# Performance work log

Hardware: AMD Instinct MI355X
Metric: run time of the kernel (lower is better)

The kernel has to match this reference:

```python
import jax, jax.numpy as jnp
import numpy as np

C_M, C_Z, H, C = 256, 128, 8, 32  # msa emb, pair emb, heads, head channels
S, R = 128, 256                   # MSA rows, residues


def layer_norm(x, gamma, beta, eps=1e-5):
    mu = jnp.mean(x, axis=-1, keepdims=True)
    var = jnp.var(x, axis=-1, keepdims=True)
    return (x - mu) * jax.lax.rsqrt(var + eps) * gamma + beta


def setup_inputs() -> dict:
    key = jax.random.key(0)
    ks = jax.random.split(key, 12)
    sc_m = 1.0 / np.sqrt(C_M)
    sc_z = 1.0 / np.sqrt(C_Z)
    sc_hc = 1.0 / np.sqrt(H * C)
    return {
        "msa_rep": jax.random.normal(ks[0], (S, R, C_M), dtype=jnp.float32),
        "pair_rep": jax.random.normal(ks[1], (R, R, C_Z), dtype=jnp.float32),
        "ln_msa_g": jnp.ones((C_M,), jnp.float32),
        "ln_msa_b": jnp.zeros((C_M,), jnp.float32),
        "ln_pair_g": jnp.ones((C_Z,), jnp.float32),
        "ln_pair_b": jnp.zeros((C_Z,), jnp.float32),
        "w_q": jax.random.normal(ks[2], (C_M, H, C), jnp.float32) * sc_m,
        "w_k": jax.random.normal(ks[3], (C_M, H, C), jnp.float32) * sc_m,
        "w_v": jax.random.normal(ks[4], (C_M, H, C), jnp.float32) * sc_m,
        "w_g": jax.random.normal(ks[5], (C_M, H, C), jnp.float32) * sc_m,
        "b_g": jnp.zeros((H, C), jnp.float32),
        "w_b": jax.random.normal(ks[6], (C_Z, H), jnp.float32) * sc_z,
        "b_b": jnp.zeros((H,), jnp.float32),
        "w_o": jax.random.normal(ks[7], (H, C, C_M), jnp.float32) * sc_hc,
        "b_o": jnp.zeros((C_M,), jnp.float32),
    }


def reference(msa_rep, pair_rep, ln_msa_g, ln_msa_b, ln_pair_g, ln_pair_b,
              w_q, w_k, w_v, w_g, b_g, w_b, b_b, w_o, b_o):
    m = layer_norm(msa_rep, ln_msa_g, ln_msa_b)                 # [S,R,C_M]
    q = jnp.einsum('src,chd->srhd', m, w_q)                     # [S,R,H,C]
    k = jnp.einsum('src,chd->srhd', m, w_k)
    v = jnp.einsum('src,chd->srhd', m, w_v)
    gates = jax.nn.sigmoid(jnp.einsum('src,chd->srhd', m, w_g) + b_g)
    # pair bias: [R,R,H] -> [H,R,R]
    z = layer_norm(pair_rep, ln_pair_g, ln_pair_b)
    b = jnp.einsum('ijc,ch->hij', z, w_b) + b_b[:, None, None]  # [H,R,R]
    logits = jnp.einsum('sqhd,skhd->shqk', q, k) / np.sqrt(C)   # [S,H,R,R]
    logits = logits + b[None]
    w = jax.nn.softmax(logits, axis=-1)
    o = jnp.einsum('shqk,skhd->sqhd', w, v)                     # [S,R,H,C]
    o = gates * o
    out = jnp.einsum('srhd,hdc->src', o, w_o) + b_o             # [S,R,C_M]
    return out
```

## Files before the change

kernel.cpp:

```cpp
#include <hip/hip_runtime.h>
#include <hip/hip_bf16.h>

#define S_DIM 128
#define R_DIM 256
#define CM 256
#define CZ 128
#define H_DIM 8
#define C_DIM 32

typedef short bf16x8 __attribute__((ext_vector_type(8)));
typedef float f32x4 __attribute__((ext_vector_type(4)));

__device__ inline ushort f2b(float f) {
  __hip_bfloat16 b = __float2bfloat16(f);
  return *(ushort*)&b;
}
__device__ inline float b2f(ushort u) {
  __hip_bfloat16 b = *(__hip_bfloat16*)&u;
  return __bfloat162float(b);
}

__device__ __forceinline__ void gld_lds16(const ushort* g, ushort* l) {
  __builtin_amdgcn_global_load_lds(
      (const __attribute__((address_space(1))) unsigned int*)g,
      (__attribute__((address_space(3))) unsigned int*)l, 16, 0, 0);
}

__global__ __launch_bounds__(256) void wt_kernel(
    const float* __restrict__ wq, const float* __restrict__ wk,
    const float* __restrict__ wv, const float* __restrict__ wg,
    const float* __restrict__ wo, ushort* __restrict__ Wt5) {
  __shared__ float t[64][65];
  int z = blockIdx.z;
  const float* W = (z == 0) ? wq : (z == 1) ? wk : (z == 2) ? wv
                   : (z == 3) ? wg : wo;
  ushort* Wt = Wt5 + (size_t)z * 65536;
  int tid = threadIdx.x;
  int r = tid >> 2, c4 = (tid & 3) * 16;
  int rowBase = blockIdx.y * 64, colBase = blockIdx.x * 64;
#pragma unroll
  for (int j = 0; j < 16; ++j)
    t[r][c4 + j] = W[(size_t)(rowBase + r) * 256 + colBase + c4 + j];
  __syncthreads();
#pragma unroll
  for (int j = 0; j < 16; ++j)
    Wt[(size_t)(colBase + r) * 256 + rowBase + c4 + j] = f2b(t[c4 + j][r]);
}

__global__ __launch_bounds__(256) void ln_msa_kernel(
    const float* __restrict__ x, const float* __restrict__ g,
    const float* __restrict__ b, ushort* __restrict__ m) {
  int lane = threadIdx.x & 63, w = threadIdx.x >> 6;
  int row = blockIdx.x * 4 + w;
  const float* xp = x + (size_t)row * CM + lane * 4;
  float4 v = *(const float4*)xp;
  float s1 = v.x + v.y + v.z + v.w;
  float s2 = v.x * v.x + v.y * v.y + v.z * v.z + v.w * v.w;
#pragma unroll
  for (int off = 32; off; off >>= 1) {
    s1 += __shfl_xor(s1, off, 64);
    s2 += __shfl_xor(s2, off, 64);
  }
  float mean = s1 * (1.0f / CM);
  float rstd = rsqrtf(s2 * (1.0f / CM) - mean * mean + 1e-5f);
  float4 gv = *(const float4*)(g + lane * 4);
  float4 bv = *(const float4*)(b + lane * 4);
  ushort4 o;
  o.x = f2b((v.x - mean) * rstd * gv.x + bv.x);
  o.y = f2b((v.y - mean) * rstd * gv.y + bv.y);
  o.z = f2b((v.z - mean) * rstd * gv.z + bv.z);
  o.w = f2b((v.w - mean) * rstd * gv.w + bv.w);
  *(ushort4*)(m + (size_t)row * CM + lane * 4) = o;
}

__global__ __launch_bounds__(256) void pair_bias_kernel(
    const float* __restrict__ z, const float* __restrict__ g,
    const float* __restrict__ b, const float* __restrict__ w_b,
    const float* __restrict__ b_b, float* __restrict__ bias) {
  __shared__ float wbs[CZ][8];
  __shared__ float gs[CZ], bs[CZ];
  int tid = threadIdx.x;
  if (tid < CZ) { gs[tid] = g[tid]; bs[tid] = b[tid]; }
  for (int i = tid; i < CZ * 8; i += 256) wbs[i >> 3][i & 7] = w_b[i];
  __syncthreads();
  int q = tid & 3;
  int row = blockIdx.x * 64 + (tid >> 2);
  const float* zp = z + (size_t)row * CZ + q * 32;
  float4 v[8];
#pragma unroll
  for (int j = 0; j < 8; ++j) v[j] = *(const float4*)(zp + j * 4);
  float s1 = 0.f, s2 = 0.f;
#pragma unroll
  for (int j = 0; j < 8; ++j) {
    s1 += v[j].x + v[j].y + v[j].z + v[j].w;
    s2 += v[j].x * v[j].x + v[j].y * v[j].y + v[j].z * v[j].z +
          v[j].w * v[j].w;
  }
  s1 += __shfl_xor(s1, 1, 64);
  s2 += __shfl_xor(s2, 1, 64);
  s1 += __shfl_xor(s1, 2, 64);
  s2 += __shfl_xor(s2, 2, 64);
  float mean = s1 * (1.0f / CZ);
  float var = s2 * (1.0f / CZ) - mean * mean;
  float rstd = rsqrtf(var + 1e-5f);
  float acc[8] = {};
#pragma unroll
  for (int j = 0; j < 8; ++j) {
    float e[4] = {v[j].x, v[j].y, v[j].z, v[j].w};
#pragma unroll
    for (int u = 0; u < 4; ++u) {
      int c = q * 32 + j * 4 + u;
      float zn = (e[u] - mean) * rstd * gs[c] + bs[c];
#pragma unroll
      for (int h = 0; h < 8; ++h) acc[h] += zn * wbs[c][h];
    }
  }
#pragma unroll
  for (int h = 0; h < 8; ++h) {
    acc[h] += __shfl_xor(acc[h], 1, 64);
    acc[h] += __shfl_xor(acc[h], 2, 64);
  }
  int h0 = q * 2;
  bias[(size_t)h0 * (R_DIM * R_DIM) + row] = acc[h0] + b_b[h0];
  bias[(size_t)(h0 + 1) * (R_DIM * R_DIM) + row] = acc[h0 + 1] + b_b[h0 + 1];
}

__global__ __launch_bounds__(256) void proj_mfma(
    const ushort* __restrict__ M, const ushort* __restrict__ Wt5,
    const float* __restrict__ b_g, ushort* __restrict__ qb,
    ushort* __restrict__ kb2, ushort* __restrict__ vb,
    ushort* __restrict__ gb) {
  __shared__ ushort As[128 * 64];
  __shared__ ushort Bs[128 * 64];
  int tid = threadIdx.x, lane = tid & 63, wid = tid >> 6;
  int lr = lane & 15, lg = lane >> 4;
  int rowBase = blockIdx.x * 128;
  int colBase = blockIdx.y * 128;
  int proj = colBase >> 8;
  int sc = (lane & 7) ^ ((lane >> 3) & 7);
  const ushort* Ag =
      M + (size_t)(rowBase + wid * 32 + (lane >> 3)) * 256 + sc * 8;
  const ushort* Bg =
      Wt5 + (size_t)(colBase + wid * 32 + (lane >> 3)) * 256 + sc * 8;
  ushort* Asl = As + wid * (32 * 64);
  ushort* Bsl = Bs + wid * (32 * 64);
  int wr = wid >> 1, wc = wid & 1;
  int sx = (lr & 7) * 8;
  f32x4 zf = {0.f, 0.f, 0.f, 0.f};
  f32x4 acc[4][4];
#pragma unroll
  for (int i = 0; i < 4; ++i)
#pragma unroll
    for (int j = 0; j < 4; ++j) acc[i][j] = zf;

  for (int kb = 0; kb < 4; ++kb) {
    if (kb) __syncthreads();
#pragma unroll
    for (int c = 0; c < 4; ++c) {
      gld_lds16(Ag + kb * 64 + c * (8 * 256), Asl + c * (8 * 64));
      gld_lds16(Bg + kb * 64 + c * (8 * 256), Bsl + c * (8 * 64));
    }
    __syncthreads();
#pragma unroll
    for (int kk = 0; kk < 2; ++kk) {
      bf16x8 a[4], b[4];
#pragma unroll
      for (int mf = 0; mf < 4; ++mf)
        a[mf] = *(const bf16x8*)&As[(wr * 64 + mf * 16 + lr) * 64 +
                                    ((kk * 32 + lg * 8) ^ sx)];
#pragma unroll
      for (int nf = 0; nf < 4; ++nf)
        b[nf] = *(const bf16x8*)&Bs[(wc * 64 + nf * 16 + lr) * 64 +
                                    ((kk * 32 + lg * 8) ^ sx)];
#pragma unroll
      for (int mf = 0; mf < 4; ++mf)
#pragma unroll
        for (int nf = 0; nf < 4; ++nf)
          acc[mf][nf] = __builtin_amdgcn_mfma_f32_16x16x32_bf16(
              a[mf], b[nf], acc[mf][nf], 0, 0, 0);
    }
  }
#pragma unroll
  for (int mf = 0; mf < 4; ++mf)
#pragma unroll
    for (int nf = 0; nf < 4; ++nf)
#pragma unroll
      for (int r = 0; r < 4; ++r) {
        int row = rowBase + wr * 64 + mf * 16 + lg * 4 + r;
        int col = (colBase & 255) + wc * 64 + nf * 16 + lr;
        int s = row >> 8, rr = row & 255, h = col >> 5, d = col & 31;
        size_t oidx = ((size_t)((s * H_DIM + h) * R_DIM + rr)) * C_DIM + d;
        float val = acc[mf][nf][r];
        if (proj == 0)
          qb[oidx] = f2b(val * 0.17677669529663687f);
        else if (proj == 1)
          kb2[oidx] = f2b(val);
        else if (proj == 2)
          vb[oidx] = f2b(val);
        else {
          val = 1.f / (1.f + __expf(-(val + b_g[col])));
          gb[oidx] = f2b(val);
        }
      }
}

__global__ __launch_bounds__(512, 4) void attn_mfma(
    const ushort* __restrict__ q, const ushort* __restrict__ k,
    const ushort* __restrict__ v, const ushort* __restrict__ g,
    const float* __restrict__ bias, ushort* __restrict__ ob) {
  __shared__ ushort Vt[32][264];
  __shared__ ushort Pl[8][32][72];
  int blk = blockIdx.x;
  int s = blk >> 3, h = blk & 7;
  int tid = threadIdx.x, lane = tid & 63, w = tid >> 6;
  int lr = lane & 15, lg = lane >> 4;
  size_t base = (size_t)(s * H_DIM + h) * (R_DIM * C_DIM);

  {
    int key = tid >> 1, half = (tid & 1) * 16;
    const ushort* vp = v + base + (size_t)key * 32 + half;
    bf16x8 t0 = *(const bf16x8*)vp;
    bf16x8 t1 = *(const bf16x8*)(vp + 8);
#pragma unroll
    for (int j = 0; j < 8; ++j) {
      Vt[half + j][key] = (ushort)t0[j];
      Vt[half + 8 + j][key] = (ushort)t1[j];
    }
  }
  __syncthreads();

  int qrow0 = w * 32;
  bf16x8 qf[2];
#pragma unroll
  for (int mf = 0; mf < 2; ++mf)
    qf[mf] = *(const bf16x8*)(q + base + (size_t)(qrow0 + mf * 16 + lr) * 32 +
                              lg * 8);
  const float* bp0 = bias + ((size_t)h * R_DIM + qrow0 + lg * 4) * R_DIM +
                     lr * 4;

  float lsum[2][4] = {};
  f32x4 of[2][2];
  f32x4 zf = {0.f, 0.f, 0.f, 0.f};
#pragma unroll
  for (int mf = 0; mf < 2; ++mf) {
    of[mf][0] = zf;
    of[mf][1] = zf;
  }

  for (int t = 0; t < 4; ++t) {
    int k0 = t * 64;
    bf16x8 kf[4];
#pragma unroll
    for (int nf = 0; nf < 4; ++nf)
      kf[nf] = *(const bf16x8*)(k + base + (size_t)(k0 + lr * 4 + nf) * 32 +
                                lg * 8);
    f32x4 sf[2][4];
#pragma unroll
    for (int mf = 0; mf < 2; ++mf)
#pragma unroll
      for (int nf = 0; nf < 4; ++nf)
        sf[mf][nf] =
            __builtin_amdgcn_mfma_f32_16x16x32_bf16(qf[mf], kf[nf], zf, 0, 0, 0);
#pragma unroll
    for (int mf = 0; mf < 2; ++mf) {
      float4 bv[4];
#pragma unroll
      for (int r = 0; r < 4; ++r)
        bv[r] = *(const float4*)(bp0 + (size_t)(mf * 16 + r) * R_DIM + k0);
#pragma unroll
      for (int r = 0; r < 4; ++r) {
        float p0 = __expf(sf[mf][0][r] + bv[r].x);
        float p1 = __expf(sf[mf][1][r] + bv[r].y);
        float p2 = __expf(sf[mf][2][r] + bv[r].z);
        float p3 = __expf(sf[mf][3][r] + bv[r].w);
        lsum[mf][r] += (p0 + p1) + (p2 + p3);
        ushort4 pk;
        pk.x = f2b(p0);
        pk.y = f2b(p1);
        pk.z = f2b(p2);
        pk.w = f2b(p3);
        *(ushort4*)&Pl[w][mf * 16 + lg * 4 + r][lr * 4] = pk;
      }
    }
#pragma unroll
    for (int kt = 0; kt < 2; ++kt) {
      bf16x8 pf[2], vf[2];
#pragma unroll
      for (int mf = 0; mf < 2; ++mf)
        pf[mf] = *(const bf16x8*)&Pl[w][mf * 16 + lr][kt * 32 + lg * 8];
#pragma unroll
      for (int df = 0; df < 2; ++df)
        vf[df] = *(const bf16x8*)&Vt[df * 16 + lr][k0 + kt * 32 + lg * 8];
#pragma unroll
      for (int mf = 0; mf < 2; ++mf)
#pragma unroll
        for (int df = 0; df < 2; ++df)
          of[mf][df] = __builtin_amdgcn_mfma_f32_16x16x32_bf16(
              pf[mf], vf[df], of[mf][df], 0, 0, 0);
    }
  }
#pragma unroll
  for (int mf = 0; mf < 2; ++mf)
#pragma unroll
    for (int r = 0; r < 4; ++r) {
#pragma unroll
      for (int msk = 1; msk <= 8; msk <<= 1)
        lsum[mf][r] += __shfl_xor(lsum[mf][r], msk, 64);
    }
#pragma unroll
  for (int mf = 0; mf < 2; ++mf)
#pragma unroll
    for (int r = 0; r < 4; ++r) {
      float inv = 1.f / lsum[mf][r];
      int row = qrow0 + mf * 16 + lg * 4 + r;
#pragma unroll
      for (int df = 0; df < 2; ++df) {
        int d = df * 16 + lr;
        float gt = b2f(g[base + (size_t)row * 32 + d]);
        ob[((size_t)(s * R_DIM + row)) * 256 + h * 32 + d] =
            f2b(of[mf][df][r] * inv * gt);
      }
    }
}

__global__ __launch_bounds__(256) void out_mfma(
    const ushort* __restrict__ A, const ushort* __restrict__ Wt,
    const float* __restrict__ b_o, float* __restrict__ out) {
  __shared__ ushort As[128 * 64];
  __shared__ ushort Bs[128 * 64];
  int tid = threadIdx.x, lane = tid & 63, wid = tid >> 6;
  int lr = lane & 15, lg = lane >> 4;
  int rowBase = blockIdx.x * 128;
  int colBase = blockIdx.y * 128;
  int sc = (lane & 7) ^ ((lane >> 3) & 7);
  const ushort* Ag =
      A + (size_t)(rowBase + wid * 32 + (lane >> 3)) * 256 + sc * 8;
  const ushort* Bg =
      Wt + (size_t)(colBase + wid * 32 + (lane >> 3)) * 256 + sc * 8;
  ushort* Asl = As + wid * (32 * 64);
  ushort* Bsl = Bs + wid * (32 * 64);
  int wr = wid >> 1, wc = wid & 1;
  int sx = (lr & 7) * 8;
  f32x4 zf = {0.f, 0.f, 0.f, 0.f};
  f32x4 acc[4][4];
#pragma unroll
  for (int i = 0; i < 4; ++i)
#pragma unroll
    for (int j = 0; j < 4; ++j) acc[i][j] = zf;

  for (int kb = 0; kb < 4; ++kb) {
    if (kb) __syncthreads();
#pragma unroll
    for (int c = 0; c < 4; ++c) {
      gld_lds16(Ag + kb * 64 + c * (8 * 256), Asl + c * (8 * 64));
      gld_lds16(Bg + kb * 64 + c * (8 * 256), Bsl + c * (8 * 64));
    }
    __syncthreads();
#pragma unroll
    for (int kk = 0; kk < 2; ++kk) {
      bf16x8 a[4], b[4];
#pragma unroll
      for (int mf = 0; mf < 4; ++mf)
        a[mf] = *(const bf16x8*)&As[(wr * 64 + mf * 16 + lr) * 64 +
                                    ((kk * 32 + lg * 8) ^ sx)];
#pragma unroll
      for (int nf = 0; nf < 4; ++nf)
        b[nf] = *(const bf16x8*)&Bs[(wc * 64 + nf * 16 + lr) * 64 +
                                    ((kk * 32 + lg * 8) ^ sx)];
#pragma unroll
      for (int mf = 0; mf < 4; ++mf)
#pragma unroll
        for (int nf = 0; nf < 4; ++nf)
          acc[mf][nf] = __builtin_amdgcn_mfma_f32_16x16x32_bf16(
              a[mf], b[nf], acc[mf][nf], 0, 0, 0);
    }
  }
#pragma unroll
  for (int mf = 0; mf < 4; ++mf)
#pragma unroll
    for (int nf = 0; nf < 4; ++nf)
#pragma unroll
      for (int r = 0; r < 4; ++r) {
        int row = rowBase + wr * 64 + mf * 16 + lg * 4 + r;
        int col = colBase + wc * 64 + nf * 16 + lr;
        out[(size_t)row * 256 + col] = acc[mf][nf][r] + b_o[col];
      }
}

extern "C" void kernel_launch(void* const* d_in, const int* in_sizes, int n_in,
                              void* d_out, int out_size, void* d_ws,
                              size_t ws_size, hipStream_t stream) {
  const float* msa      = (const float*)d_in[0];
  const float* pair     = (const float*)d_in[1];
  const float* ln_msa_g = (const float*)d_in[2];
  const float* ln_msa_b = (const float*)d_in[3];
  const float* ln_pr_g  = (const float*)d_in[4];
  const float* ln_pr_b  = (const float*)d_in[5];
  const float* w_q      = (const float*)d_in[6];
  const float* w_k      = (const float*)d_in[7];
  const float* w_v      = (const float*)d_in[8];
  const float* w_g      = (const float*)d_in[9];
  const float* b_g      = (const float*)d_in[10];
  const float* w_b      = (const float*)d_in[11];
  const float* b_b      = (const float*)d_in[12];
  const float* w_o      = (const float*)d_in[13];
  const float* b_o      = (const float*)d_in[14];
  float* out = (float*)d_out;

  char* ws = (char*)d_ws;
  ushort* m   = (ushort*)(ws + 0);
  ushort* qb  = (ushort*)(ws + 16777216ull);
  ushort* kb  = (ushort*)(ws + 33554432ull);
  ushort* vb  = (ushort*)(ws + 50331648ull);
  ushort* gb  = (ushort*)(ws + 67108864ull);
  float*  bi  = (float*) (ws + 83886080ull);
  ushort* ob  = (ushort*)(ws + 85983232ull);
  ushort* Wt5 = (ushort*)(ws + 102760448ull);

  wt_kernel<<<dim3(4, 4, 5), 256, 0, stream>>>(w_q, w_k, w_v, w_g, w_o, Wt5);
  ln_msa_kernel<<<S_DIM * R_DIM / 4, 256, 0, stream>>>(msa, ln_msa_g,
                                                       ln_msa_b, m);
  pair_bias_kernel<<<R_DIM * R_DIM / 64, 256, 0, stream>>>(
      pair, ln_pr_g, ln_pr_b, w_b, b_b, bi);
  proj_mfma<<<dim3(256, 8), 256, 0, stream>>>(m, Wt5, b_g, qb, kb, vb, gb);
  attn_mfma<<<S_DIM * H_DIM, 512, 0, stream>>>(qb, kb, vb, gb, bi, ob);
  out_mfma<<<dim3(256, 2), 256, 0, stream>>>(ob, Wt5 + 4 * 65536, b_o, out);
}
```

Measured before the change: 137.5 us.

## Double-buffer LDS tiles in projection and output GEMMs to overlap loads with MFMA

Both bf16 GEMM kernels (QKVG projection and output projection) now keep two LDS buffers per operand. The next K-slice is prefetched with global_load_lds while MFMAs run on the current one, using explicit vmcnt waits and s_barrier calls. This hides global-load latency that the old load-sync-compute loop exposed. LDS use doubles to 64 KB per block, which may cut occupancy, and the extra barrier per iteration adds sync cost.

```diff
diff --git a/kernel.cpp b/kernel.cpp
--- a/kernel.cpp
+++ b/kernel.cpp
@@ -130,8 +130,8 @@
     const float* __restrict__ b_g, ushort* __restrict__ qb,
     ushort* __restrict__ kb2, ushort* __restrict__ vb,
     ushort* __restrict__ gb) {
-  __shared__ ushort As[128 * 64];
-  __shared__ ushort Bs[128 * 64];
+  __shared__ ushort As[2][128 * 64];
+  __shared__ ushort Bs[2][128 * 64];
   int tid = threadIdx.x, lane = tid & 63, wid = tid >> 6;
   int lr = lane & 15, lg = lane >> 4;
   int rowBase = blockIdx.x * 128;
@@ -142,8 +142,7 @@
       M + (size_t)(rowBase + wid * 32 + (lane >> 3)) * 256 + sc * 8;
   const ushort* Bg =
       Wt5 + (size_t)(colBase + wid * 32 + (lane >> 3)) * 256 + sc * 8;
-  ushort* Asl = As + wid * (32 * 64);
-  ushort* Bsl = Bs + wid * (32 * 64);
+  int ldsOff = wid * (32 * 64);
   int wr = wid >> 1, wc = wid & 1;
   int sx = (lr & 7) * 8;
   f32x4 zf = {0.f, 0.f, 0.f, 0.f};
@@ -153,25 +152,40 @@
 #pragma unroll
     for (int j = 0; j < 4; ++j) acc[i][j] = zf;
 
+#pragma unroll
+  for (int c = 0; c < 4; ++c) {
+    gld_lds16(Ag + c * (8 * 256), &As[0][ldsOff + c * (8 * 64)]);
+    gld_lds16(Bg + c * (8 * 256), &Bs[0][ldsOff + c * (8 * 64)]);
+  }
+#pragma unroll
   for (int kb = 0; kb < 4; ++kb) {
-    if (kb) __syncthreads();
-#pragma unroll
-    for (int c = 0; c < 4; ++c) {
-      gld_lds16(Ag + kb * 64 + c * (8 * 256), Asl + c * (8 * 64));
-      gld_lds16(Bg + kb * 64 + c * (8 * 256), Bsl + c * (8 * 64));
-    }
-    __syncthreads();
+    int cur = kb & 1;
+    if (kb < 3) {
+#pragma unroll
+      for (int c = 0; c < 4; ++c) {
+        gld_lds16(Ag + (kb + 1) * 64 + c * (8 * 256),
+                  &As[cur ^ 1][ldsOff + c * (8 * 64)]);
+        gld_lds16(Bg + (kb + 1) * 64 + c * (8 * 256),
+                  &Bs[cur ^ 1][ldsOff + c * (8 * 64)]);
+      }
+      asm volatile("s_waitcnt vmcnt(8)" ::: "memory");
+    } else {
+      asm volatile("s_waitcnt vmcnt(0)" ::: "memory");
+    }
+    __builtin_amdgcn_sched_barrier(0);
+    __builtin_amdgcn_s_barrier();
+    __builtin_amdgcn_sched_barrier(0);
 #pragma unroll
     for (int kk = 0; kk < 2; ++kk) {
       bf16x8 a[4], b[4];
 #pragma unroll
       for (int mf = 0; mf < 4; ++mf)
-        a[mf] = *(const bf16x8*)&As[(wr * 64 + mf * 16 + lr) * 64 +
-                                    ((kk * 32 + lg * 8) ^ sx)];
+        a[mf] = *(const bf16x8*)&As[cur][(wr * 64 + mf * 16 + lr) * 64 +
+                                         ((kk * 32 + lg * 8) ^ sx)];
 #pragma unroll
       for (int nf = 0; nf < 4; ++nf)
-        b[nf] = *(const bf16x8*)&Bs[(wc * 64 + nf * 16 + lr) * 64 +
-                                    ((kk * 32 + lg * 8) ^ sx)];
+        b[nf] = *(const bf16x8*)&Bs[cur][(wc * 64 + nf * 16 + lr) * 64 +
+                                         ((kk * 32 + lg * 8) ^ sx)];
 #pragma unroll
       for (int mf = 0; mf < 4; ++mf)
 #pragma unroll
@@ -179,6 +193,9 @@
           acc[mf][nf] = __builtin_amdgcn_mfma_f32_16x16x32_bf16(
               a[mf], b[nf], acc[mf][nf], 0, 0, 0);
     }
+    __builtin_amdgcn_sched_barrier(0);
+    __builtin_amdgcn_s_barrier();
+    __builtin_amdgcn_sched_barrier(0);
   }
 #pragma unroll
   for (int mf = 0; mf < 4; ++mf)
@@ -326,8 +343,8 @@
 __global__ __launch_bounds__(256) void out_mfma(
     const ushort* __restrict__ A, const ushort* __restrict__ Wt,
     const float* __restrict__ b_o, float* __restrict__ out) {
-  __shared__ ushort As[128 * 64];
-  __shared__ ushort Bs[128 * 64];
+  __shared__ ushort As[2][128 * 64];
+  __shared__ ushort Bs[2][128 * 64];
   int tid = threadIdx.x, lane = tid & 63, wid = tid >> 6;
   int lr = lane & 15, lg = lane >> 4;
   int rowBase = blockIdx.x * 128;
@@ -337,8 +354,7 @@
       A + (size_t)(rowBase + wid * 32 + (lane >> 3)) * 256 + sc * 8;
   const ushort* Bg =
       Wt + (size_t)(colBase + wid * 32 + (lane >> 3)) * 256 + sc * 8;
-  ushort* Asl = As + wid * (32 * 64);
-  ushort* Bsl = Bs + wid * (32 * 64);
+  int ldsOff = wid * (32 * 64);
   int wr = wid >> 1, wc = wid & 1;
   int sx = (lr & 7) * 8;
   f32x4 zf = {0.f, 0.f, 0.f, 0.f};
@@ -348,25 +364,40 @@
 #pragma unroll
     for (int j = 0; j < 4; ++j) acc[i][j] = zf;
 
+#pragma unroll
+  for (int c = 0; c < 4; ++c) {
+    gld_lds16(Ag + c * (8 * 256), &As[0][ldsOff + c * (8 * 64)]);
+    gld_lds16(Bg + c * (8 * 256), &Bs[0][ldsOff + c * (8 * 64)]);
+  }
+#pragma unroll
   for (int kb = 0; kb < 4; ++kb) {
-    if (kb) __syncthreads();
-#pragma unroll
-    for (int c = 0; c < 4; ++c) {
-      gld_lds16(Ag + kb * 64 + c * (8 * 256), Asl + c * (8 * 64));
-      gld_lds16(Bg + kb * 64 + c * (8 * 256), Bsl + c * (8 * 64));
-    }
-    __syncthreads();
+    int cur = kb & 1;
+    if (kb < 3) {
+#pragma unroll
+      for (int c = 0; c < 4; ++c) {
+        gld_lds16(Ag + (kb + 1) * 64 + c * (8 * 256),
+                  &As[cur ^ 1][ldsOff + c * (8 * 64)]);
+        gld_lds16(Bg + (kb + 1) * 64 + c * (8 * 256),
+                  &Bs[cur ^ 1][ldsOff + c * (8 * 64)]);
+      }
+      asm volatile("s_waitcnt vmcnt(8)" ::: "memory");
+    } else {
+      asm volatile("s_waitcnt vmcnt(0)" ::: "memory");
+    }
+    __builtin_amdgcn_sched_barrier(0);
+    __builtin_amdgcn_s_barrier();
+    __builtin_amdgcn_sched_barrier(0);
 #pragma unroll
     for (int kk = 0; kk < 2; ++kk) {
       bf16x8 a[4], b[4];
 #pragma unroll
       for (int mf = 0; mf < 4; ++mf)
-        a[mf] = *(const bf16x8*)&As[(wr * 64 + mf * 16 + lr) * 64 +
-                                    ((kk * 32 + lg * 8) ^ sx)];
+        a[mf] = *(const bf16x8*)&As[cur][(wr * 64 + mf * 16 + lr) * 64 +
+                                         ((kk * 32 + lg * 8) ^ sx)];
 #pragma unroll
       for (int nf = 0; nf < 4; ++nf)
-        b[nf] = *(const bf16x8*)&Bs[(wc * 64 + nf * 16 + lr) * 64 +
-                                    ((kk * 32 + lg * 8) ^ sx)];
+        b[nf] = *(const bf16x8*)&Bs[cur][(wc * 64 + nf * 16 + lr) * 64 +
+                                         ((kk * 32 + lg * 8) ^ sx)];
 #pragma unroll
       for (int mf = 0; mf < 4; ++mf)
 #pragma unroll
@@ -374,6 +405,9 @@
           acc[mf][nf] = __builtin_amdgcn_mfma_f32_16x16x32_bf16(
               a[mf], b[nf], acc[mf][nf], 0, 0, 0);
     }
+    __builtin_amdgcn_sched_barrier(0);
+    __builtin_amdgcn_s_barrier();
+    __builtin_amdgcn_sched_barrier(0);
   }
 #pragma unroll
   for (int mf = 0; mf < 4; ++mf)
```

New measurement: 139.6 us. No clear change (+1.5%).
